# Kernel tuning notes

Measured on AMD Instinct MI355X. Metric: run time of the kernel, lower is better.

The kernel has to match this reference:

```python
import jax, jax.numpy as jnp
import numpy as np

CAPACITY = 1024


def setup_inputs() -> dict:
    T, H, I, E, K = 2048, 1024, 1408, 8, 2
    key = jax.random.key(0)
    k0, k1, k2, k3, k4 = jax.random.split(key, 5)
    hidden_states = jax.random.normal(k0, (T, H), dtype=jnp.float32)
    w1 = jax.random.normal(k1, (E, 2 * I, H), dtype=jnp.float32) * 0.02  # [gate; up]
    w2 = jax.random.normal(k2, (E, H, I), dtype=jnp.float32) * 0.02
    topk_weights = jax.random.uniform(k3, (T, K), dtype=jnp.float32)
    topk_ids = jax.random.randint(k4, (T, K), 0, E, dtype=jnp.int32)
    return {"hidden_states": hidden_states, "w1": w1, "w2": w2,
            "topk_weights": topk_weights, "topk_ids": topk_ids}


def reference(hidden_states, w1, w2, topk_weights, topk_ids):
    # MoE: prepare(dispatch) -> grouped expert GEMM (silu-gated MLP) -> finalize(combine)
    T, H = hidden_states.shape
    E = w1.shape[0]
    I = w2.shape[2]
    K = topk_ids.shape[1]
    C = CAPACITY

    # ---- prepare: dispatch token copies to per-expert buffers ----
    flat_ids = topk_ids.reshape(-1)                       # (T*K,)
    onehot = jax.nn.one_hot(flat_ids, E, dtype=jnp.int32)  # (T*K, E)
    cs = jnp.cumsum(onehot, axis=0)                        # running per-expert counts
    pos = jnp.take_along_axis(cs, flat_ids[:, None], axis=1)[:, 0] - 1  # slot in expert buffer
    keep = pos < C
    pos_c = jnp.where(keep, pos, 0)

    x_flat = jnp.repeat(hidden_states, K, axis=0)          # (T*K, H)
    x_e = jnp.zeros((E, C, H), dtype=hidden_states.dtype)
    x_e = x_e.at[flat_ids, pos_c].add(jnp.where(keep[:, None], x_flat, 0.0))

    # ---- grouped expert GEMM: silu(gate) * up, then down-proj ----
    h = jnp.einsum('ech,eoh->eco', x_e, w1)                # (E, C, 2I)
    gate, up = h[..., :I], h[..., I:]
    act = jax.nn.silu(gate) * up                           # (E, C, I)
    y = jnp.einsum('eci,ehi->ech', act, w2)                # (E, C, H)

    # ---- finalize: gather back, apply router weights, reduce over top-k ----
    y_flat = y[flat_ids, pos_c] * (keep[:, None].astype(y.dtype)) \
             * topk_weights.reshape(-1, 1)                 # (T*K, H)
    out = y_flat.reshape(T, K, H).sum(axis=1)              # (T, H)
    return out.astype(hidden_states.dtype)
```

## Files before the change

kernel.cpp:

```cpp
#include <hip/hip_runtime.h>

#define NE 8
#define CAP 1024
#define HD 1024
#define ID 1408
#define TT 2048

typedef __attribute__((ext_vector_type(8))) short bf16x8;
typedef __attribute__((ext_vector_type(4))) float f32x4;
typedef unsigned short u16;
typedef unsigned int u32;

__device__ __forceinline__ u16 f2bf(float f) {
  u32 u = __float_as_uint(f);
  u = (u + 0x7fffu + ((u >> 16) & 1u)) >> 16;
  return (u16)u;
}
__device__ __forceinline__ float bf2f(u16 b) {
  return __uint_as_float(((u32)b) << 16);
}

__device__ __forceinline__ void async_cp16(const void* g, void* l) {
  __builtin_amdgcn_global_load_lds(
      (const __attribute__((address_space(1))) u32*)g,
      (__attribute__((address_space(3))) u32*)l, 16, 0, 0);
}

__global__ void cvt_kernel(const float4* __restrict__ src, ushort4* __restrict__ dst, int n4) {
  int i = blockIdx.x * 256 + threadIdx.x;
  if (i >= n4) return;
  float4 v = src[i];
  ushort4 o;
  o.x = f2bf(v.x); o.y = f2bf(v.y); o.z = f2bf(v.z); o.w = f2bf(v.w);
  dst[i] = o;
}

__global__ void route_kernel(const int* __restrict__ ids, int* __restrict__ rowmap,
                             int* __restrict__ flatpos, int* __restrict__ counts) {
  __shared__ int ids_s[TT * 2];
  __shared__ int lc[256][NE];
  int tid = threadIdx.x;
  for (int i = tid; i < TT * 2; i += 256) ids_s[i] = ids[i];
#pragma unroll
  for (int e = 0; e < NE; ++e) lc[tid][e] = 0;
  __syncthreads();
  int base = tid * 16;
#pragma unroll
  for (int j = 0; j < 16; ++j) lc[tid][ids_s[base + j]]++;
  __syncthreads();
  if (tid < NE) {
    int run = 0;
    for (int t = 0; t < 256; ++t) { int v = lc[t][tid]; lc[t][tid] = run; run += v; }
    counts[tid] = run < CAP ? run : CAP;
  }
  __syncthreads();
#pragma unroll
  for (int j = 0; j < 16; ++j) {
    int f = base + j;
    int e = ids_s[f];
    int p = lc[tid][e]++;
    if (p < CAP) { rowmap[e * CAP + p] = f; flatpos[f] = p; }
    else flatpos[f] = -1;
  }
}

template <bool GATHER>
__global__ __launch_bounds__(256) void gemm_bt(
    const u16* __restrict__ A, const u16* __restrict__ B, u16* __restrict__ C,
    const int* __restrict__ rowmap, const int* __restrict__ counts,
    int KE, int Astride, long long Bexp, int Cstride) {
  int e = blockIdx.z;
  int count = counts[e];
  int m0 = blockIdx.y * 128;
  if (m0 >= count) return;
  int n0 = blockIdx.x * 128;
  int tid = threadIdx.x;
  int lane = tid & 63, wid = tid >> 6;
  int wm = wid >> 1, wn = wid & 1;
  int q = lane >> 4, lm = lane & 15;

  __shared__ __align__(16) char smA[128 * 128];
  __shared__ __align__(16) char smB[128 * 128];

  int rloc = tid >> 3;
  int chs = ((tid & 7) ^ (rloc & 7)) * 8;
  const u16* aP[4];
  const u16* bP[4];
#pragma unroll
  for (int i = 0; i < 4; ++i) {
    int row = rloc + 32 * i;
    if (GATHER) {
      int gr = m0 + row;
      int f = (gr < count) ? rowmap[e * CAP + gr] : 0;
      aP[i] = A + (size_t)(f >> 1) * Astride + chs;
    } else {
      aP[i] = A + ((size_t)e * CAP + m0 + row) * Astride + chs;
    }
    bP[i] = B + (size_t)e * Bexp + (size_t)(n0 + row) * KE + chs;
  }

  f32x4 zero = {0.f, 0.f, 0.f, 0.f};
  f32x4 acc[4][4];
#pragma unroll
  for (int mi = 0; mi < 4; ++mi)
#pragma unroll
    for (int ni = 0; ni < 4; ++ni) acc[mi][ni] = zero;

  int nkt = KE >> 6;
  for (int kt = 0; kt < nkt; ++kt) {
    int ko = kt * 64;
#pragma unroll
    for (int i = 0; i < 4; ++i) {
      async_cp16(aP[i] + ko, smA + (i * 256 + tid) * 16);
      async_cp16(bP[i] + ko, smB + (i * 256 + tid) * 16);
    }
    asm volatile("s_waitcnt vmcnt(0)" ::: "memory");
    __syncthreads();
#pragma unroll
    for (int s = 0; s < 2; ++s) {
      bf16x8 af[4], bfr[4];
#pragma unroll
      for (int mi = 0; mi < 4; ++mi) {
        int row = wm * 64 + mi * 16 + lm;
        af[mi] = *(const bf16x8*)(smA + row * 128 + (((s * 4 + q) ^ (lm & 7)) * 16));
      }
#pragma unroll
      for (int ni = 0; ni < 4; ++ni) {
        int row = wn * 64 + ni * 16 + lm;
        bfr[ni] = *(const bf16x8*)(smB + row * 128 + (((s * 4 + q) ^ (lm & 7)) * 16));
      }
#pragma unroll
      for (int mi = 0; mi < 4; ++mi)
#pragma unroll
        for (int ni = 0; ni < 4; ++ni)
          acc[mi][ni] = __builtin_amdgcn_mfma_f32_16x16x32_bf16(af[mi], bfr[ni], acc[mi][ni], 0, 0, 0);
    }
    __syncthreads();
  }

#pragma unroll
  for (int mi = 0; mi < 4; ++mi) {
#pragma unroll
    for (int ni = 0; ni < 4; ++ni) {
      int col = n0 + wn * 64 + ni * 16 + lm;
#pragma unroll
      for (int r = 0; r < 4; ++r) {
        int row = m0 + wm * 64 + mi * 16 + q * 4 + r;
        C[((size_t)e * CAP + row) * Cstride + col] = f2bf(acc[mi][ni][r]);
      }
    }
  }
}

struct alignas(16) us8 { u16 v[8]; };
__global__ void act_kernel(u16* __restrict__ h, const int* __restrict__ counts) {
  int e = blockIdx.y;
  int c = blockIdx.x;
  if (c >= counts[e]) return;
  int tid = threadIdx.x;
  if (tid >= ID / 8) return;
  u16* rowp = h + ((size_t)e * CAP + c) * (2 * ID);
  us8 g = *(const us8*)(rowp + tid * 8);
  us8 u = *(const us8*)(rowp + ID + tid * 8);
  us8 o;
#pragma unroll
  for (int j = 0; j < 8; ++j) {
    float gf = bf2f(g.v[j]);
    float uf = bf2f(u.v[j]);
    float a = gf / (1.f + __expf(-gf)) * uf;
    o.v[j] = f2bf(a);
  }
  *(us8*)(rowp + tid * 8) = o;
}

__global__ void combine_kernel(const float* __restrict__ tw, const int* __restrict__ ids,
                               const int* __restrict__ flatpos, const u16* __restrict__ y,
                               float* __restrict__ out) {
  int t = blockIdx.x;
  int tid = threadIdx.x;
  int h0 = tid * 4;
  float a0 = 0.f, a1 = 0.f, a2 = 0.f, a3 = 0.f;
#pragma unroll
  for (int k = 0; k < 2; ++k) {
    int f = t * 2 + k;
    int p = flatpos[f];
    if (p >= 0) {
      int e = ids[f];
      float w = tw[f];
      const u16* yr = y + ((size_t)e * CAP + p) * HD + h0;
      ushort4 v = *(const ushort4*)yr;
      a0 += w * bf2f(v.x);
      a1 += w * bf2f(v.y);
      a2 += w * bf2f(v.z);
      a3 += w * bf2f(v.w);
    }
  }
  float4 o = {a0, a1, a2, a3};
  *(float4*)(out + (size_t)t * HD + h0) = o;
}

extern "C" void kernel_launch(void* const* d_in, const int* in_sizes, int n_in,
                              void* d_out, int out_size, void* d_ws, size_t ws_size,
                              hipStream_t stream) {
  const float* hidden = (const float*)d_in[0];
  const float* w1 = (const float*)d_in[1];
  const float* w2 = (const float*)d_in[2];
  const float* tw = (const float*)d_in[3];
  const int* ids = (const int*)d_in[4];
  float* out = (float*)d_out;

  char* p = (char*)d_ws;
  auto alloc = [&](size_t b) { char* r = p; p += (b + 255) & ~(size_t)255; return r; };
  u16* bw1 = (u16*)alloc((size_t)NE * 2 * ID * HD * 2);
  u16* bw2 = (u16*)alloc((size_t)NE * HD * ID * 2);
  u16* bx = (u16*)alloc((size_t)TT * HD * 2);
  u16* hbuf = (u16*)alloc((size_t)NE * CAP * 2 * ID * 2);
  u16* ybuf = (u16*)alloc((size_t)NE * CAP * HD * 2);
  int* rowmap = (int*)alloc((size_t)NE * CAP * 4);
  int* flatpos = (int*)alloc((size_t)TT * 2 * 4);
  int* counts = (int*)alloc((size_t)NE * 4);

  int n4w1 = NE * 2 * ID * HD / 4;
  cvt_kernel<<<(n4w1 + 255) / 256, 256, 0, stream>>>((const float4*)w1, (ushort4*)bw1, n4w1);
  int n4w2 = NE * HD * ID / 4;
  cvt_kernel<<<(n4w2 + 255) / 256, 256, 0, stream>>>((const float4*)w2, (ushort4*)bw2, n4w2);
  int n4x = TT * HD / 4;
  cvt_kernel<<<(n4x + 255) / 256, 256, 0, stream>>>((const float4*)hidden, (ushort4*)bx, n4x);

  route_kernel<<<1, 256, 0, stream>>>(ids, rowmap, flatpos, counts);

  gemm_bt<true><<<dim3(2 * ID / 128, CAP / 128, NE), 256, 0, stream>>>(
      bx, bw1, hbuf, rowmap, counts, HD, HD, (long long)2 * ID * HD, 2 * ID);

  act_kernel<<<dim3(CAP, NE), 256, 0, stream>>>(hbuf, counts);

  gemm_bt<false><<<dim3(HD / 128, CAP / 128, NE), 256, 0, stream>>>(
      hbuf, bw2, ybuf, rowmap, counts, ID, 2 * ID, (long long)HD * ID, HD);

  combine_kernel<<<TT, 256, 0, stream>>>(tw, ids, flatpos, ybuf, out);
}
```

Measured before the change: 289.7 us.

## Parallelize routing prefix scan and reorder GEMM grid to interleave experts

The routing kernel replaces its serial 256-step per-expert scan (run by only 8 threads) with a packed 64-bit histogram per thread followed by a parallel Hillis-Steele scan over all 256 threads. The GEMM grids now put the expert index on blockIdx.x and the N tile on blockIdx.z, so consecutive workgroups cover different experts instead of many N tiles of one expert. The aim is to cut the latency of the single-block route kernel and to change dispatch order, which may spread early-exiting empty tiles more evenly. The cost is B-weight locality, since neighbouring blocks now read different experts' weights, which could hurt L2 reuse.

```diff
diff --git a/kernel.cpp b/kernel.cpp
--- a/kernel.cpp
+++ b/kernel.cpp
@@ -10,6 +10,7 @@
 typedef __attribute__((ext_vector_type(4))) float f32x4;
 typedef unsigned short u16;
 typedef unsigned int u32;
+typedef unsigned long long u64;
 
 __device__ __forceinline__ u16 f2bf(float f) {
   u32 u = __float_as_uint(f);
@@ -38,27 +39,46 @@
 __global__ void route_kernel(const int* __restrict__ ids, int* __restrict__ rowmap,
                              int* __restrict__ flatpos, int* __restrict__ counts) {
   __shared__ int ids_s[TT * 2];
-  __shared__ int lc[256][NE];
+  __shared__ int sc[256][NE + 1];
   int tid = threadIdx.x;
   for (int i = tid; i < TT * 2; i += 256) ids_s[i] = ids[i];
-#pragma unroll
-  for (int e = 0; e < NE; ++e) lc[tid][e] = 0;
   __syncthreads();
   int base = tid * 16;
-#pragma unroll
-  for (int j = 0; j < 16; ++j) lc[tid][ids_s[base + j]]++;
+  u64 own64 = 0;
+#pragma unroll
+  for (int j = 0; j < 16; ++j) own64 += 1ull << (ids_s[base + j] * 8);
+  int own[NE];
+#pragma unroll
+  for (int e = 0; e < NE; ++e) { own[e] = (int)((own64 >> (e * 8)) & 0xff); sc[tid][e] = own[e]; }
   __syncthreads();
-  if (tid < NE) {
-    int run = 0;
-    for (int t = 0; t < 256; ++t) { int v = lc[t][tid]; lc[t][tid] = run; run += v; }
-    counts[tid] = run < CAP ? run : CAP;
-  }
+  for (int off = 1; off < 256; off <<= 1) {
+    int v[NE];
+    if (tid >= off) {
+#pragma unroll
+      for (int e = 0; e < NE; ++e) v[e] = sc[tid - off][e];
+    }
+    __syncthreads();
+    if (tid >= off) {
+#pragma unroll
+      for (int e = 0; e < NE; ++e) sc[tid][e] += v[e];
+    }
+    __syncthreads();
+  }
+  if (tid == 255) {
+#pragma unroll
+    for (int e = 0; e < NE; ++e) counts[e] = sc[255][e] < CAP ? sc[255][e] : CAP;
+  }
+  int excl[NE];
+#pragma unroll
+  for (int e = 0; e < NE; ++e) excl[e] = sc[tid][e] - own[e];
   __syncthreads();
+#pragma unroll
+  for (int e = 0; e < NE; ++e) sc[tid][e] = excl[e];
 #pragma unroll
   for (int j = 0; j < 16; ++j) {
     int f = base + j;
     int e = ids_s[f];
-    int p = lc[tid][e]++;
+    int p = sc[tid][e]++;
     if (p < CAP) { rowmap[e * CAP + p] = f; flatpos[f] = p; }
     else flatpos[f] = -1;
   }
@@ -69,11 +89,11 @@
     const u16* __restrict__ A, const u16* __restrict__ B, u16* __restrict__ C,
     const int* __restrict__ rowmap, const int* __restrict__ counts,
     int KE, int Astride, long long Bexp, int Cstride) {
-  int e = blockIdx.z;
+  int e = blockIdx.x;
   int count = counts[e];
   int m0 = blockIdx.y * 128;
   if (m0 >= count) return;
-  int n0 = blockIdx.x * 128;
+  int n0 = blockIdx.z * 128;
   int tid = threadIdx.x;
   int lane = tid & 63, wid = tid >> 6;
   int wm = wid >> 1, wn = wid & 1;
@@ -229,12 +249,12 @@
 
   route_kernel<<<1, 256, 0, stream>>>(ids, rowmap, flatpos, counts);
 
-  gemm_bt<true><<<dim3(2 * ID / 128, CAP / 128, NE), 256, 0, stream>>>(
+  gemm_bt<true><<<dim3(NE, CAP / 128, 2 * ID / 128), 256, 0, stream>>>(
       bx, bw1, hbuf, rowmap, counts, HD, HD, (long long)2 * ID * HD, 2 * ID);
 
   act_kernel<<<dim3(CAP, NE), 256, 0, stream>>>(hbuf, counts);
 
-  gemm_bt<false><<<dim3(HD / 128, CAP / 128, NE), 256, 0, stream>>>(
+  gemm_bt<false><<<dim3(NE, CAP / 128, HD / 128), 256, 0, stream>>>(
       hbuf, bw2, ybuf, rowmap, counts, ID, 2 * ID, (long long)HD * ID, HD);
 
   combine_kernel<<<TT, 256, 0, stream>>>(tw, ids, flatpos, ybuf, out);
```

After: 289.2 us. Within noise of the previous version (-0.2%).
